# Optimization experiments

Measured on AMD Instinct MI355X. Metric: run time of the kernel, lower is better.

## Reference

```python
import jax, jax.numpy as jnp
import numpy as np

OUT_F = 4096
IN_F = 4096
NNZ_PER_ROW = 205            # ortho_ratio 0.05 * IN_F
NNZ = OUT_F * NNZ_PER_ROW    # 839680
ALPHA = 1.0                  # self.alpha (privacy on)


def setup_inputs() -> dict:
    key = jax.random.key(0)
    k1, k2, k3, k4 = jax.random.split(key, 4)
    x = jax.random.normal(k1, (4, 2048, IN_F), dtype=jnp.float32)
    # offset-uint8 quantized weight (stored here as int32 in [0,256))
    base_packed = jax.random.randint(k2, (OUT_F, IN_F), 0, 256, dtype=jnp.int32)
    # per-output-row dequant scales (robust_max/127 -> small positive values)
    scales = jax.random.uniform(k3, (OUT_F,), dtype=jnp.float32, minval=1e-4, maxval=4e-3)
    # CSR sparse residual: uniform row occupancy, sorted col indices per row
    ortho_vals = (jax.random.normal(k4, (NNZ,), dtype=jnp.float32) * 0.01).astype(jnp.float16)
    rng = np.random.default_rng(0)
    cols = np.sort(rng.integers(0, IN_F, size=(OUT_F, NNZ_PER_ROW)), axis=1)
    ortho_indices = jnp.asarray(cols.reshape(-1).astype(np.int32))
    ortho_ptr = jnp.asarray((np.arange(OUT_F + 1) * NNZ_PER_ROW).astype(np.int32))
    return {
        "x": x,
        "base_packed": base_packed,
        "scales": scales,
        "ortho_vals": ortho_vals,
        "ortho_indices": ortho_indices,
        "ortho_ptr": ortho_ptr,
    }


def reference(x, base_packed, scales, ortho_vals, ortho_indices, ortho_ptr):
    orig_shape = x.shape
    x_flat = x.reshape(-1, IN_F).astype(jnp.float32)          # [T, IN_F]
    # dequantize int8 base weight: (u8 - 128) * scale_row
    w_base = (base_packed.astype(jnp.float32) - 128.0) * scales[:, None]  # [OUT_F, IN_F]
    # expand CSR row pointers -> per-nnz row ids (fixed total length, jit-safe)
    counts = jnp.diff(ortho_ptr)
    rows = jnp.repeat(jnp.arange(OUT_F, dtype=jnp.int32), counts,
                      total_repeat_length=ortho_vals.shape[0])
    # scatter sparse residual into dense weight (matches torch CSR->dense fallback)
    w_ortho = jnp.zeros((OUT_F, IN_F), jnp.float32).at[rows, ortho_indices].add(
        ortho_vals.astype(jnp.float32))
    w = w_base + ALPHA * w_ortho
    out = x_flat @ w.T                                         # [T, OUT_F]
    return out.reshape(orig_shape[:-1] + (OUT_F,)).astype(x.dtype)
```

## Files before the change

kernel.cpp:

```cpp
#include <hip/hip_runtime.h>
#include <hip/hip_fp16.h>

#define IN_F 4096
#define OUT_F 4096
#define TOK 8192
#define NNZ_PER_ROW 205
#define NNZ (OUT_F * NNZ_PER_ROW)

typedef __attribute__((ext_vector_type(8))) _Float16 f16x8;
typedef __attribute__((ext_vector_type(4))) float floatx4;


__global__ __launch_bounds__(256) void cvt_x_kernel(const float* __restrict__ x,
                                                    _Float16* __restrict__ xh) {
    int t = blockIdx.x * 256 + threadIdx.x;
    const float4* p = (const float4*)x + (size_t)t * 2;
    float4 a = p[0], b = p[1];
    f16x8 h;
    h[0] = (_Float16)a.x; h[1] = (_Float16)a.y; h[2] = (_Float16)a.z; h[3] = (_Float16)a.w;
    h[4] = (_Float16)b.x; h[5] = (_Float16)b.y; h[6] = (_Float16)b.z; h[7] = (_Float16)b.w;
    ((f16x8*)xh)[t] = h;
}

__global__ __launch_bounds__(256) void dequant_w_kernel(const int* __restrict__ bp,
                                                        const float* __restrict__ scales,
                                                        _Float16* __restrict__ wh) {
    int t = blockIdx.x * 256 + threadIdx.x;
    int row = t >> 9;
    float s = scales[row];
    const int4* p = (const int4*)bp + (size_t)t * 2;
    int4 a = p[0], b = p[1];
    f16x8 h;
    h[0] = (_Float16)((float)(a.x - 128) * s);
    h[1] = (_Float16)((float)(a.y - 128) * s);
    h[2] = (_Float16)((float)(a.z - 128) * s);
    h[3] = (_Float16)((float)(a.w - 128) * s);
    h[4] = (_Float16)((float)(b.x - 128) * s);
    h[5] = (_Float16)((float)(b.y - 128) * s);
    h[6] = (_Float16)((float)(b.z - 128) * s);
    h[7] = (_Float16)((float)(b.w - 128) * s);
    ((f16x8*)wh)[t] = h;
}

__global__ __launch_bounds__(256) void sparse_add_kernel(const void* __restrict__ vals_raw,
                                                         const int* __restrict__ cols,
                                                         _Float16* __restrict__ wh) {
    int k = blockIdx.x * 256 + threadIdx.x;
    if (k >= NNZ) return;

    const float*    vf = (const float*)vals_raw;
    const _Float16* vh = (const _Float16*)vals_raw;
    float mx = 0.f;
    for (int i = 0; i < 64; ++i) {
        float a = __builtin_fabsf(vf[i]);
        mx = a > mx ? a : mx;
    }
    const bool is_f32 = (mx > 1e-6f) && (mx < 1.0f);

    int row  = k / NNZ_PER_ROW;
    int rbeg = row * NNZ_PER_ROW;
    int rend = rbeg + NNZ_PER_ROW;
    int c    = cols[k];
    if (k != rbeg && cols[k - 1] == c) return;

    float s = is_f32 ? vf[k] : (float)vh[k];
    for (int k2 = k + 1; k2 < rend && cols[k2] == c; ++k2)
        s += is_f32 ? vf[k2] : (float)vh[k2];

    _Float16* p = wh + (size_t)row * IN_F + c;
    *p = (_Float16)((float)*p + s);
}


__global__ __launch_bounds__(512, 2) void gemm256_kernel(const _Float16* __restrict__ X,
                                                         const _Float16* __restrict__ W,
                                                         float* __restrict__ out) {
    extern __shared__ char smem[];
    const int tid  = threadIdx.x;
    const int lane = tid & 63;
    const int w    = tid >> 6;
    const int wm   = w >> 2;
    const int wn   = w & 3;

    const int bid = blockIdx.x;
    const int swz = (bid & 7) * 64 + (bid >> 3);
    const int bm  = swz >> 4;
    const int bn  = swz & 15;

    const _Float16* Ap = X + (size_t)(bm * 256) * IN_F;
    const _Float16* Bp = W + (size_t)(bn * 256) * IN_F;

    const int l8 = lane >> 3;
    const int e  = (lane & 7) ^ l8;

    auto stage = [&](const _Float16* panel, int ldsBase, int rowBase, int kcol) {
#pragma unroll
        for (int j = 0; j < 2; ++j) {
            int ch = w * 2 + j;
            const _Float16* gp = panel + (size_t)(rowBase + ch * 8 + l8) * IN_F + kcol + e * 8;
            char* lp = smem + ldsBase + ch * 1024;
            __builtin_amdgcn_global_load_lds(
                (const __attribute__((address_space(1))) void*)gp,
                (__attribute__((address_space(3))) void*)lp, 16, 0, 0);
        }
    };

    const int q     = lane >> 4;
    const int r15   = lane & 15;
    const int slot0 = (q ^ (r15 & 7)) * 16;

    floatx4 acc[8][4] = {};
    f16x8 afrag[4], bfrag[4];

#define LOAD_B(KKH) do {                                                        \
    const char* Bb = smem + buf + 32768;                                        \
    _Pragma("unroll")                                                           \
    for (int nt = 0; nt < 4; ++nt)                                              \
        bfrag[nt] = *(const f16x8*)(Bb + (wn * 64 + nt * 16 + r15) * 128        \
                                       + (slot0 ^ ((KKH) * 64)));               \
} while (0)

#define LOAD_A(MQ, KKH) do {                                                    \
    const char* Ab = smem + buf;                                                \
    _Pragma("unroll")                                                           \
    for (int mt = 0; mt < 4; ++mt)                                              \
        afrag[mt] = *(const f16x8*)(Ab + (wm * 128 + (MQ) * 64 + mt * 16 + r15) * 128 \
                                       + (slot0 ^ ((KKH) * 64)));               \
} while (0)

#define MFMA_BLK(MQ) do {                                                       \
    __builtin_amdgcn_s_setprio(1);                                              \
    _Pragma("unroll")                                                           \
    for (int mt = 0; mt < 4; ++mt)                                              \
        _Pragma("unroll")                                                       \
        for (int nt = 0; nt < 4; ++nt)                                          \
            acc[(MQ) * 4 + mt][nt] = __builtin_amdgcn_mfma_f32_16x16x32_f16(    \
                afrag[mt], bfrag[nt], acc[(MQ) * 4 + mt][nt], 0, 0, 0);         \
    __builtin_amdgcn_s_setprio(0);                                              \
} while (0)

    stage(Bp, 32768, 0, 0);
    stage(Bp, 49152, 128, 0);
    stage(Ap, 0, 0, 0);
    stage(Ap, 16384, 128, 0);
    stage(Bp, 65536 + 32768, 0, 64);
    stage(Bp, 65536 + 49152, 128, 64);
    asm volatile("s_waitcnt vmcnt(4)" ::: "memory");
    __builtin_amdgcn_s_barrier();

    for (int kt = 0; kt < 64; ++kt) {
        const int buf = (kt & 1) << 16;
        const int ob  = ((kt + 1) & 1) << 16;

        LOAD_B(0);
        LOAD_A(0, 0);
        if (kt < 63) stage(Ap, ob, 0, (kt + 1) * 64);
        __builtin_amdgcn_s_barrier();
        MFMA_BLK(0);
        __builtin_amdgcn_s_barrier();

        LOAD_A(1, 0);
        if (kt < 63) stage(Ap, ob + 16384, 128, (kt + 1) * 64);
        __builtin_amdgcn_s_barrier();
        MFMA_BLK(1);
        __builtin_amdgcn_s_barrier();

        LOAD_B(1);
        LOAD_A(0, 1);
        __builtin_amdgcn_s_barrier();
        MFMA_BLK(0);
        __builtin_amdgcn_s_barrier();

        LOAD_A(1, 1);
        if (kt < 62) {
            stage(Bp, buf + 32768, 0, (kt + 2) * 64);
            stage(Bp, buf + 49152, 128, (kt + 2) * 64);
        }
        __builtin_amdgcn_s_barrier();
        MFMA_BLK(1);
        if (kt < 62)       asm volatile("s_waitcnt vmcnt(4)" ::: "memory");
        else if (kt == 62) asm volatile("s_waitcnt vmcnt(0)" ::: "memory");
        __builtin_amdgcn_s_barrier();
    }

#undef LOAD_B
#undef LOAD_A
#undef MFMA_BLK

#pragma unroll
    for (int mq = 0; mq < 2; ++mq)
#pragma unroll
        for (int mt = 0; mt < 4; ++mt)
#pragma unroll
            for (int nt = 0; nt < 4; ++nt) {
                const int o    = bn * 256 + wn * 64 + nt * 16 + r15;
                const int trow = bm * 256 + wm * 128 + mq * 64 + mt * 16 + q * 4;
                const floatx4 v = acc[mq * 4 + mt][nt];
#pragma unroll
                for (int r = 0; r < 4; ++r)
                    out[(size_t)(trow + r) * OUT_F + o] = v[r];
            }
}


__global__ __launch_bounds__(256) void gemm_fast_kernel(const _Float16* __restrict__ X,
                                                        const _Float16* __restrict__ W,
                                                        float* __restrict__ out) {
    __shared__ __align__(1024) char smem[32768];
    const int tid  = threadIdx.x;
    const int lane = tid & 63;
    const int w    = tid >> 6;
    const int wm   = w >> 1;
    const int wn   = w & 1;
    const int bm   = blockIdx.y;
    const int bn   = blockIdx.x;

    const int l8 = lane >> 3;
    const int ls = lane & 7;
    const int e  = ls ^ l8;

    floatx4 acc[4][4] = {};

    for (int k0 = 0; k0 < IN_F; k0 += 64) {
#pragma unroll
        for (int j = 0; j < 4; ++j) {
            int c   = w * 4 + j;
            int row = c * 8 + l8;
            const _Float16* gp = X + ((size_t)(bm * 128 + row)) * IN_F + k0 + e * 8;
            char* lp = smem + c * 1024;
            __builtin_amdgcn_global_load_lds((const __attribute__((address_space(1))) void*)gp,
                                             (__attribute__((address_space(3))) void*)lp,
                                             16, 0, 0);
        }
#pragma unroll
        for (int j = 0; j < 4; ++j) {
            int c   = w * 4 + j;
            int row = c * 8 + l8;
            const _Float16* gp = W + ((size_t)(bn * 128 + row)) * IN_F + k0 + e * 8;
            char* lp = smem + 16384 + c * 1024;
            __builtin_amdgcn_global_load_lds((const __attribute__((address_space(1))) void*)gp,
                                             (__attribute__((address_space(3))) void*)lp,
                                             16, 0, 0);
        }
        __syncthreads();

        const int q   = lane >> 4;
        const int r15 = lane & 15;
#pragma unroll
        for (int kk = 0; kk < 64; kk += 32) {
            int j = (kk >> 3) + q;
            f16x8 a[4], b[4];
#pragma unroll
            for (int mt = 0; mt < 4; ++mt) {
                int row = wm * 64 + mt * 16 + r15;
                a[mt] = *(const f16x8*)(smem + row * 128 + ((j ^ (row & 7)) * 16));
            }
#pragma unroll
            for (int nt = 0; nt < 4; ++nt) {
                int row = wn * 64 + nt * 16 + r15;
                b[nt] = *(const f16x8*)(smem + 16384 + row * 128 + ((j ^ (row & 7)) * 16));
            }
#pragma unroll
            for (int mt = 0; mt < 4; ++mt)
#pragma unroll
                for (int nt = 0; nt < 4; ++nt)
                    acc[mt][nt] = __builtin_amdgcn_mfma_f32_16x16x32_f16(a[mt], b[nt],
                                                                         acc[mt][nt], 0, 0, 0);
        }
        __syncthreads();
    }

    const int q   = lane >> 4;
    const int r15 = lane & 15;
#pragma unroll
    for (int mt = 0; mt < 4; ++mt)
#pragma unroll
        for (int nt = 0; nt < 4; ++nt) {
            int o     = bn * 128 + wn * 64 + nt * 16 + r15;
            int tbase = bm * 128 + wm * 64 + mt * 16 + q * 4;
#pragma unroll
            for (int r = 0; r < 4; ++r)
                out[(size_t)(tbase + r) * OUT_F + o] = acc[mt][nt][r];
        }
}

__global__ __launch_bounds__(256) void gemm_kernel(const float* __restrict__ X,
                                                   const _Float16* __restrict__ W,
                                                   float* __restrict__ out) {
    __shared__ __align__(16) _Float16 As[128 * 72];
    __shared__ __align__(16) _Float16 Bs[128 * 72];
    const int tid  = threadIdx.x;
    const int lane = tid & 63;
    const int w    = tid >> 6;
    const int wm   = w >> 1;
    const int wn   = w & 1;
    const int bm   = blockIdx.y;
    const int bn   = blockIdx.x;
    const int srow = tid >> 3;
    const int sch  = tid & 7;

    const float*    Xb = X + (size_t)(bm * 128) * IN_F;
    const _Float16* Wb = W + (size_t)(bn * 128) * IN_F;

    floatx4 acc[4][4] = {};

    for (int k0 = 0; k0 < IN_F; k0 += 64) {
#pragma unroll
        for (int p = 0; p < 4; ++p) {
            int row = p * 32 + srow;
            const float* gp = Xb + (size_t)row * IN_F + k0 + sch * 8;
            float4 u = ((const float4*)gp)[0];
            float4 v = ((const float4*)gp)[1];
            f16x8 h;
            h[0] = (_Float16)u.x; h[1] = (_Float16)u.y;
            h[2] = (_Float16)u.z; h[3] = (_Float16)u.w;
            h[4] = (_Float16)v.x; h[5] = (_Float16)v.y;
            h[6] = (_Float16)v.z; h[7] = (_Float16)v.w;
            *(f16x8*)&As[row * 72 + sch * 8] = h;
        }
#pragma unroll
        for (int p = 0; p < 4; ++p) {
            int row = p * 32 + srow;
            *(f16x8*)&Bs[row * 72 + sch * 8] =
                *(const f16x8*)(Wb + (size_t)row * IN_F + k0 + sch * 8);
        }
        __syncthreads();

        const int q   = lane >> 4;
        const int r15 = lane & 15;
#pragma unroll
        for (int kk = 0; kk < 64; kk += 32) {
            int j = (kk >> 3) + q;
            f16x8 a[4], b[4];
#pragma unroll
            for (int mt = 0; mt < 4; ++mt) {
                int row = wm * 64 + mt * 16 + r15;
                a[mt] = *(const f16x8*)&As[row * 72 + j * 8];
            }
#pragma unroll
            for (int nt = 0; nt < 4; ++nt) {
                int row = wn * 64 + nt * 16 + r15;
                b[nt] = *(const f16x8*)&Bs[row * 72 + j * 8];
            }
#pragma unroll
            for (int mt = 0; mt < 4; ++mt)
#pragma unroll
                for (int nt = 0; nt < 4; ++nt)
                    acc[mt][nt] = __builtin_amdgcn_mfma_f32_16x16x32_f16(a[mt], b[nt],
                                                                         acc[mt][nt], 0, 0, 0);
        }
        __syncthreads();
    }

    const int q   = lane >> 4;
    const int r15 = lane & 15;
#pragma unroll
    for (int mt = 0; mt < 4; ++mt)
#pragma unroll
        for (int nt = 0; nt < 4; ++nt) {
            int o     = bn * 128 + wn * 64 + nt * 16 + r15;
            int tbase = bm * 128 + wm * 64 + mt * 16 + q * 4;
#pragma unroll
            for (int r = 0; r < 4; ++r)
                out[(size_t)(tbase + r) * OUT_F + o] = acc[mt][nt][r];
        }
}


extern "C" void kernel_launch(void* const* d_in, const int* in_sizes, int n_in,
                              void* d_out, int out_size, void* d_ws, size_t ws_size,
                              hipStream_t stream) {
    const float* x      = (const float*)d_in[0];
    const int*   bp     = (const int*)d_in[1];
    const float* scales = (const float*)d_in[2];
    const void*  vals   = (const void*)d_in[3];
    const int*   cols   = (const int*)d_in[4];
    float*       out    = (float*)d_out;

    _Float16* wh = (_Float16*)d_ws;
    const size_t wh_bytes = (size_t)OUT_F * IN_F * 2;
    const size_t xh_bytes = (size_t)TOK * IN_F * 2;

    static int use256 = -1;
    if (use256 < 0) {
        hipError_t e = hipFuncSetAttribute((const void*)gemm256_kernel,
                                           hipFuncAttributeMaxDynamicSharedMemorySize,
                                           131072);
        use256 = (e == hipSuccess) ? 1 : 0;
    }

    dequant_w_kernel<<<OUT_F * IN_F / 8 / 256, 256, 0, stream>>>(bp, scales, wh);
    sparse_add_kernel<<<(NNZ + 255) / 256, 256, 0, stream>>>(vals, cols, wh);

    if (ws_size >= wh_bytes + xh_bytes) {
        _Float16* xh = (_Float16*)((char*)d_ws + wh_bytes);
        cvt_x_kernel<<<TOK * IN_F / 8 / 256, 256, 0, stream>>>(x, xh);
        if (use256) {
            gemm256_kernel<<<dim3(512), 512, 131072, stream>>>(xh, wh, out);
        } else {
            dim3 grid(OUT_F / 128, TOK / 128);
            gemm_fast_kernel<<<grid, 256, 0, stream>>>(xh, wh, out);
        }
    } else {
        dim3 grid(OUT_F / 128, TOK / 128);
        gemm_kernel<<<grid, 256, 0, stream>>>(x, wh, out);
    }
}
```

Before: 524.0 us.

## Double-buffer register fragments to overlap LDS reads with MFMA blocks

Splits the A/B register fragments into two sets so the LDS reads for the next MFMA block are issued while the current block's MFMAs run. This halves the barriers per k-step and adds sched_barrier fences to keep the interleaving. The global-load waits change from a partial vmcnt(4) to full vmcnt(0) drains, which may expose global load latency. More live fragment registers could also add VGPR pressure.

```diff
diff --git a/kernel.cpp b/kernel.cpp
--- a/kernel.cpp
+++ b/kernel.cpp
@@ -110,32 +110,32 @@
     const int slot0 = (q ^ (r15 & 7)) * 16;
 
     floatx4 acc[8][4] = {};
-    f16x8 afrag[4], bfrag[4];
-
-#define LOAD_B(KKH) do {                                                        \
-    const char* Bb = smem + buf + 32768;                                        \
+    f16x8 sa0[4], sa1[4], sb0[4], sb1[4];
+
+#define DS_A(DST, MQ, KKH, BUFOFF) do {                                         \
+    const char* Ab_ = smem + (BUFOFF);                                          \
+    _Pragma("unroll")                                                           \
+    for (int mt = 0; mt < 4; ++mt)                                              \
+        DST[mt] = *(const f16x8*)(Ab_ + (wm * 128 + (MQ) * 64 + mt * 16 + r15) * 128 \
+                                      + (slot0 ^ ((KKH) * 64)));                \
+} while (0)
+
+#define DS_B(DST, KKH, BUFOFF) do {                                             \
+    const char* Bb_ = smem + (BUFOFF) + 32768;                                  \
     _Pragma("unroll")                                                           \
     for (int nt = 0; nt < 4; ++nt)                                              \
-        bfrag[nt] = *(const f16x8*)(Bb + (wn * 64 + nt * 16 + r15) * 128        \
-                                       + (slot0 ^ ((KKH) * 64)));               \
+        DST[nt] = *(const f16x8*)(Bb_ + (wn * 64 + nt * 16 + r15) * 128         \
+                                      + (slot0 ^ ((KKH) * 64)));                \
 } while (0)
 
-#define LOAD_A(MQ, KKH) do {                                                    \
-    const char* Ab = smem + buf;                                                \
-    _Pragma("unroll")                                                           \
-    for (int mt = 0; mt < 4; ++mt)                                              \
-        afrag[mt] = *(const f16x8*)(Ab + (wm * 128 + (MQ) * 64 + mt * 16 + r15) * 128 \
-                                       + (slot0 ^ ((KKH) * 64)));               \
-} while (0)
-
-#define MFMA_BLK(MQ) do {                                                       \
+#define MFMA4(SA, SB, MQ) do {                                                  \
     __builtin_amdgcn_s_setprio(1);                                              \
     _Pragma("unroll")                                                           \
     for (int mt = 0; mt < 4; ++mt)                                              \
         _Pragma("unroll")                                                       \
         for (int nt = 0; nt < 4; ++nt)                                          \
             acc[(MQ) * 4 + mt][nt] = __builtin_amdgcn_mfma_f32_16x16x32_f16(    \
-                afrag[mt], bfrag[nt], acc[(MQ) * 4 + mt][nt], 0, 0, 0);         \
+                SA[mt], SB[nt], acc[(MQ) * 4 + mt][nt], 0, 0, 0);               \
     __builtin_amdgcn_s_setprio(0);                                              \
 } while (0)
 
@@ -145,47 +145,50 @@
     stage(Ap, 16384, 128, 0);
     stage(Bp, 65536 + 32768, 0, 64);
     stage(Bp, 65536 + 49152, 128, 64);
-    asm volatile("s_waitcnt vmcnt(4)" ::: "memory");
+    asm volatile("s_waitcnt vmcnt(0)" ::: "memory");
     __builtin_amdgcn_s_barrier();
+    DS_A(sa0, 0, 0, 0);
+    DS_B(sb0, 0, 0);
 
     for (int kt = 0; kt < 64; ++kt) {
         const int buf = (kt & 1) << 16;
-        const int ob  = ((kt + 1) & 1) << 16;
-
-        LOAD_B(0);
-        LOAD_A(0, 0);
+        const int ob  = buf ^ 65536;
+
+        DS_A(sa1, 1, 0, buf);
         if (kt < 63) stage(Ap, ob, 0, (kt + 1) * 64);
+        __builtin_amdgcn_sched_barrier(0);
+        MFMA4(sa0, sb0, 0);
         __builtin_amdgcn_s_barrier();
-        MFMA_BLK(0);
+
+        DS_A(sa0, 0, 1, buf);
+        DS_B(sb1, 1, buf);
+        if (kt < 63) stage(Ap, ob + 16384, 128, (kt + 1) * 64);
+        __builtin_amdgcn_sched_barrier(0);
+        MFMA4(sa1, sb0, 1);
         __builtin_amdgcn_s_barrier();
 
-        LOAD_A(1, 0);
-        if (kt < 63) stage(Ap, ob + 16384, 128, (kt + 1) * 64);
+        DS_A(sa1, 1, 1, buf);
+        __builtin_amdgcn_sched_barrier(0);
+        MFMA4(sa0, sb1, 0);
+        asm volatile("s_waitcnt vmcnt(0)" ::: "memory");
         __builtin_amdgcn_s_barrier();
-        MFMA_BLK(1);
-        __builtin_amdgcn_s_barrier();
-
-        LOAD_B(1);
-        LOAD_A(0, 1);
-        __builtin_amdgcn_s_barrier();
-        MFMA_BLK(0);
-        __builtin_amdgcn_s_barrier();
-
-        LOAD_A(1, 1);
+
+        if (kt < 63) {
+            DS_A(sa0, 0, 0, ob);
+            DS_B(sb0, 0, ob);
+        }
         if (kt < 62) {
             stage(Bp, buf + 32768, 0, (kt + 2) * 64);
             stage(Bp, buf + 49152, 128, (kt + 2) * 64);
         }
+        __builtin_amdgcn_sched_barrier(0);
+        MFMA4(sa1, sb1, 1);
         __builtin_amdgcn_s_barrier();
-        MFMA_BLK(1);
-        if (kt < 62)       asm volatile("s_waitcnt vmcnt(4)" ::: "memory");
-        else if (kt == 62) asm volatile("s_waitcnt vmcnt(0)" ::: "memory");
-        __builtin_amdgcn_s_barrier();
-    }
-
-#undef LOAD_B
-#undef LOAD_A
-#undef MFMA_BLK
+    }
+
+#undef DS_A
+#undef DS_B
+#undef MFMA4
 
 #pragma unroll
     for (int mq = 0; mq < 2; ++mq)
```

New measurement: 506.8 us. -3.3%, faster.
